# Kernel tuning notes

Measured on AMD Instinct MI355X. Metric: run time of the kernel, lower is better.

## Reference

```python
import jax, jax.numpy as jnp
import numpy as np

B, N, L = 32, 131072, 10
NUM_NEG_RATIO = 3
UP_CONF = 0.8
LO_CONF = 0.3
UP_IOU = 0.5
LO_IOU = 0.35
REG_COEFF = 1.0
MAX_OBJS = 10


def bboxes_iou_cxcywh(a, b):
    # a: [N,4], b: [L,4], boxes as (cx, cy, w, h) -> IoU matrix [N, L]
    tl = jnp.maximum(a[:, None, :2] - a[:, None, 2:] * 0.5,
                     b[None, :, :2] - b[None, :, 2:] * 0.5)
    br = jnp.minimum(a[:, None, :2] + a[:, None, 2:] * 0.5,
                     b[None, :, :2] + b[None, :, 2:] * 0.5)
    area_a = a[:, 2] * a[:, 3]
    area_b = b[:, 2] * b[:, 3]
    en = jnp.all(tl < br, axis=2)
    wh = br - tl
    area_i = wh[..., 0] * wh[..., 1] * en
    return area_i / (area_a[:, None] + area_b[None, :] - area_i)


def setup_inputs() -> dict:
    key = jax.random.key(0)
    k1, k2, k3, k4, k5 = jax.random.split(key, 5)
    logits = jax.random.normal(k1, (B, N)) * 2.0
    cxy = jax.random.uniform(k2, (B, N, 2), minval=0.0, maxval=4096.0)
    wh = jax.random.uniform(k3, (B, N, 2), minval=16.0, maxval=128.0)
    outputs = jnp.concatenate([cxy, wh, logits[..., None]], axis=-1)
    # plant L high-confidence priors per image whose boxes are jittered gt copies
    gidx = (jnp.arange(L) + 1) * 997
    outputs = outputs.at[:, gidx, 4].set(3.0)  # sigmoid(3) ~ 0.95 > 0.8
    jit_xy = jax.random.uniform(k4, (B, L, 2), minval=-3.0, maxval=3.0)
    jit_wh = jax.random.uniform(k5, (B, L, 2), minval=0.95, maxval=1.05)
    labels = jnp.concatenate([outputs[:, gidx, :2] + jit_xy,
                              outputs[:, gidx, 2:4] * jit_wh], axis=-1)
    labels = labels.at[:, 8:, 3].set(0.0)  # h==0 sentinel -> 8 valid gts per image
    return {"labels": labels, "outputs": outputs}


def _per_image(out, label):
    # out: [N,5], label: [L,4]
    logit = out[:, 4]
    conf = jax.nn.sigmoid(jax.lax.stop_gradient(logit))
    pcoords = jax.lax.stop_gradient(out[:, :4])
    h = label[:, 3]
    zero = h == 0.0
    last_idx = jnp.where(jnp.any(zero), jnp.argmax(zero), L)
    gt_valid = jnp.arange(L) < last_idx
    upper = conf > UP_CONF
    lower = conf < LO_CONF
    iou = bboxes_iou_cxcywh(pcoords, jax.lax.stop_gradient(label))  # [N,L]
    neg_inf = -jnp.inf
    iou_up = jnp.where(upper[:, None], iou, neg_inf)
    pos_ious = iou_up.max(axis=0)          # [L]
    pos_prior = iou_up.argmax(axis=0)      # [L] index into full prior dim
    neg_ious = jnp.where(lower[:, None], iou, neg_inf).max(axis=0)  # [L]
    gt_sel = gt_valid & (pos_ious >= UP_IOU)
    num_pos = gt_sel.sum()
    valid = (last_idx <= MAX_OBJS) & jnp.any(upper) & jnp.any(lower) & (num_pos > 0)
    # positive conf loss: BCEWithLogits target 1 -> softplus(-x)
    conf_pos = jnp.where(gt_sel, jax.nn.softplus(-logit[pos_prior]), 0.0).sum()
    # negatives (faithful to source quirk: gt indices index into thold_lower list)
    cs = jnp.cumsum(lower)
    match = lower[None, :] & (cs[None, :] == (jnp.arange(L) + 1)[:, None])  # [L,N]
    first_lower = jnp.argmax(match, axis=1)  # j-th lowest-index low-conf prior
    neg_cand = gt_valid & (neg_ious <= LO_IOU)
    cand_conf = jnp.where(neg_cand, conf[first_lower], neg_inf)
    rank = jnp.argsort(jnp.argsort(-cand_conf))
    neg_sel = neg_cand & (rank < NUM_NEG_RATIO * num_pos)
    # negative conf loss: target 0 -> softplus(x)
    conf_neg = jnp.where(neg_sel, jax.nn.softplus(logit[first_lower]), 0.0).sum()
    conf_loss = conf_pos + conf_neg
    pos_gt = label[:, :4]
    pred_box = out[pos_prior, :4]
    d = pred_box - pos_gt
    ad = jnp.abs(d)
    sl1 = jnp.where(ad < 1.0, 0.5 * d * d, ad - 0.5)
    max_lens = jnp.max(pos_gt[:, 2:4], axis=1, keepdims=True)
    max_lens = jnp.where(max_lens == 0.0, 1.0, max_lens)
    reg_loss = jnp.where(gt_sel[:, None], sl1 / max_lens, 0.0).sum()
    vf = valid.astype(out.dtype)
    return vf * conf_loss, vf * reg_loss, jnp.where(valid, num_pos, 0)


def reference(labels, outputs):
    conf_l, reg_l, npos = jax.vmap(_per_image)(outputs, labels)
    pos_selected = npos.sum()
    conf_loss = conf_l.sum()
    reg_loss = reg_l.sum()
    pos_f = jnp.maximum(pos_selected, 1).astype(outputs.dtype)
    ok = pos_selected >= 1
    total = jnp.where(ok, (conf_loss + REG_COEFF * reg_loss) / pos_f, 0.0)
    c = jnp.where(ok, conf_loss / pos_f, 0.0)
    r = jnp.where(ok, reg_loss / pos_f, 0.0)
    p = jnp.where(ok, pos_selected, 0).astype(outputs.dtype)
    return jnp.stack([total, c, r, p])
```

## Files before the change

kernel.cpp:

```cpp
#include <hip/hip_runtime.h>
#include <math.h>

#pragma clang fp contract(off)

#define BB 32
#define NN 131072
#define LL 10

constexpr int CHUNKS = 64;
constexpr int BLOCK  = 256;
constexpr int PER_CHUNK = NN / CHUNKS;
constexpr int GG = 4;
constexpr int ITERS = PER_CHUNK / (BLOCK * GG);

constexpr double UPPER_T =  1.3862943611198906;
constexpr double LOWER_T = -0.8472978603872034;

__device__ __forceinline__ unsigned int ordf(float f) {
    unsigned int b = __float_as_uint(f);
    return (b & 0x80000000u) ? ~b : (b | 0x80000000u);
}
__device__ __forceinline__ float unordf(unsigned int u) {
    unsigned int b = (u & 0x80000000u) ? (u & 0x7FFFFFFFu) : ~u;
    return __uint_as_float(b);
}
__device__ __forceinline__ unsigned long long shfl_xor_u64(unsigned long long v, int m) {
    int lo = __shfl_xor((int)(unsigned int)v, m, 64);
    int hi = __shfl_xor((int)(unsigned int)(v >> 32), m, 64);
    return ((unsigned long long)(unsigned int)hi << 32) | (unsigned long long)(unsigned int)lo;
}
__device__ __forceinline__ float softplusf(float x) {
    return fmaxf(x, 0.0f) + log1pf(expf(-fabsf(x)));
}

__global__ __launch_bounds__(BLOCK) void reduce_kernel(
    const float* __restrict__ outputs, const float* __restrict__ labels,
    unsigned long long* __restrict__ up_keys, unsigned int* __restrict__ lo_keys,
    unsigned int* __restrict__ flags)
{
    const int img   = blockIdx.x / CHUNKS;
    const int chunk = blockIdx.x % CHUNKS;
    const float* img_out = outputs + (size_t)img * NN * 5;

    __shared__ float sb[LL][5];
    __shared__ unsigned long long s_up[4][LL];
    __shared__ unsigned int s_lo[4][LL];
    __shared__ unsigned int s_flag;

    const int t = threadIdx.x;
    if (t < LL) {
        const float* lb = labels + ((size_t)img * LL + t) * 4;
        float cx = lb[0], cy = lb[1], w = lb[2], h = lb[3];
        sb[t][0] = cx - w * 0.5f;
        sb[t][1] = cy - h * 0.5f;
        sb[t][2] = cx + w * 0.5f;
        sb[t][3] = cy + h * 0.5f;
        sb[t][4] = w * h;
    }
    if (t == 0) s_flag = 0;
    __syncthreads();

    unsigned long long bu[LL];
    unsigned int bl[LL];
    #pragma unroll
    for (int j = 0; j < LL; ++j) { bu[j] = 0ull; bl[j] = 0u; }
    unsigned int myflag = 0;

    const int base = chunk * PER_CHUNK;
    #pragma unroll
    for (int it = 0; it < ITERS; ++it) {
        const int p0 = base + (it * BLOCK + t) * GG;
        const float4* src = (const float4*)(img_out + (size_t)p0 * 5);
        float4 v0 = src[0], v1 = src[1], v2 = src[2], v3 = src[3], v4 = src[4];
        float px[4] = { v0.x, v1.y, v2.z, v3.w };
        float py[4] = { v0.y, v1.z, v2.w, v4.x };
        float pw[4] = { v0.z, v1.w, v3.x, v4.y };
        float ph[4] = { v0.w, v2.x, v3.y, v4.z };
        float pl[4] = { v1.x, v2.y, v3.z, v4.w };
        #pragma unroll
        for (int g = 0; g < GG; ++g) {
            float logit = pl[g];
            bool up = (double)logit > UPPER_T;
            bool lo = (double)logit < LOWER_T;
            if (up) myflag |= 1u;
            if (lo) myflag |= 2u;
            if (up || lo) {
                float atlx = px[g] - pw[g] * 0.5f;
                float atly = py[g] - ph[g] * 0.5f;
                float abrx = px[g] + pw[g] * 0.5f;
                float abry = py[g] + ph[g] * 0.5f;
                float aa   = pw[g] * ph[g];
                unsigned int idx = (unsigned int)(p0 + g);
                #pragma unroll
                for (int j = 0; j < LL; ++j) {
                    float tlx = fmaxf(atlx, sb[j][0]);
                    float tly = fmaxf(atly, sb[j][1]);
                    float brx = fminf(abrx, sb[j][2]);
                    float bry = fminf(abry, sb[j][3]);
                    bool en = (tlx < brx) && (tly < bry);
                    float ai = en ? (brx - tlx) * (bry - tly) : 0.0f;
                    float iou = ai / (aa + sb[j][4] - ai);
                    unsigned int ub = ordf(iou);
                    if (up) {
                        unsigned long long key =
                            ((unsigned long long)ub << 32) | (unsigned long long)(0xFFFFFFFFu - idx);
                        if (key > bu[j]) bu[j] = key;
                    }
                    if (lo) {
                        if (ub > bl[j]) bl[j] = ub;
                    }
                }
            }
        }
    }

    const int wid = t >> 6;
    #pragma unroll
    for (int j = 0; j < LL; ++j) {
        unsigned long long v = bu[j];
        unsigned int u = bl[j];
        #pragma unroll
        for (int m = 1; m < 64; m <<= 1) {
            unsigned long long v2 = shfl_xor_u64(v, m);
            if (v2 > v) v = v2;
            unsigned int u2 = (unsigned int)__shfl_xor((int)u, m, 64);
            if (u2 > u) u = u2;
        }
        if ((t & 63) == 0) { s_up[wid][j] = v; s_lo[wid][j] = u; }
    }
    #pragma unroll
    for (int m = 1; m < 64; m <<= 1)
        myflag |= (unsigned int)__shfl_xor((int)myflag, m, 64);
    if ((t & 63) == 0) atomicOr(&s_flag, myflag);
    __syncthreads();

    if (t < LL) {
        unsigned long long m = s_up[0][t];
        #pragma unroll
        for (int w = 1; w < 4; ++w) if (s_up[w][t] > m) m = s_up[w][t];
        if (m) atomicMax(&up_keys[img * LL + t], m);
    } else if (t < 2 * LL) {
        int j = t - LL;
        unsigned int m = s_lo[0][j];
        #pragma unroll
        for (int w = 1; w < 4; ++w) if (s_lo[w][j] > m) m = s_lo[w][j];
        if (m) atomicMax(&lo_keys[img * LL + j], m);
    } else if (t == 2 * LL) {
        if (s_flag) atomicOr(&flags[img], s_flag);
    }
}

__global__ __launch_bounds__(64) void epilogue_kernel(
    const float* __restrict__ outputs, const float* __restrict__ labels,
    const unsigned long long* __restrict__ up_keys, const unsigned int* __restrict__ lo_keys,
    const unsigned int* __restrict__ flags,
    float* __restrict__ res_conf, float* __restrict__ res_reg, int* __restrict__ res_np)
{
    const int img  = blockIdx.x;
    const int lane = threadIdx.x;
    const float* po = outputs + (size_t)img * NN * 5;

    int fl[LL];
    #pragma unroll
    for (int j = 0; j < LL; ++j) fl[j] = 0;
    int cnt = 0;
    for (int k = 0; k < NN / 64 && cnt < LL; ++k) {
        float lg = po[(size_t)(k * 64 + lane) * 5 + 4];
        bool lo = (double)lg < LOWER_T;
        unsigned long long m = __ballot(lo);
        while (m && cnt < LL) {
            int b = __builtin_ctzll(m);
            fl[cnt++] = k * 64 + b;
            m &= (m - 1);
        }
    }
    if (lane != 0) return;

    float pos_iou[LL]; int pos_prior[LL]; float neg_iou[LL];
    for (int j = 0; j < LL; ++j) {
        unsigned long long key = up_keys[img * LL + j];
        if (key == 0ull) { pos_iou[j] = -INFINITY; pos_prior[j] = 0; }
        else {
            pos_iou[j]   = unordf((unsigned int)(key >> 32));
            pos_prior[j] = (int)(0xFFFFFFFFu - (unsigned int)key);
        }
        unsigned int lk = lo_keys[img * LL + j];
        neg_iou[j] = (lk == 0u) ? -INFINITY : unordf(lk);
    }

    const float* plab = labels + (size_t)img * LL * 4;
    int last_idx = LL;
    for (int j = 0; j < LL; ++j) {
        if (plab[j * 4 + 3] == 0.0f) { last_idx = j; break; }
    }

    bool gt_sel[LL]; int num_pos = 0;
    for (int j = 0; j < LL; ++j) {
        gt_sel[j] = (j < last_idx) && (pos_iou[j] >= 0.5f);
        num_pos += gt_sel[j] ? 1 : 0;
    }

    unsigned int f = flags[img];
    bool valid = (last_idx <= 10) && ((f & 1u) != 0) && ((f & 2u) != 0) && (num_pos > 0);

    float conf_pos = 0.0f;
    for (int j = 0; j < LL; ++j) {
        if (gt_sel[j]) {
            float lg = po[(size_t)pos_prior[j] * 5 + 4];
            conf_pos += softplusf(-lg);
        }
    }

    bool nc[LL]; float cl[LL];
    for (int j = 0; j < LL; ++j) {
        nc[j] = (j < last_idx) && (neg_iou[j] <= 0.35f);
        cl[j] = po[(size_t)fl[j] * 5 + 4];
    }

    float conf_neg = 0.0f;
    for (int j = 0; j < LL; ++j) {
        if (!nc[j]) continue;
        float cj = cl[j];
        int rank = 0;
        for (int k = 0; k < LL; ++k) {
            if (!nc[k]) continue;
            float ck = cl[k];
            if (ck > cj || (ck == cj && k < j)) rank++;
        }
        if (rank < 3 * num_pos) conf_neg += softplusf(cj);
    }

    float reg = 0.0f;
    for (int j = 0; j < LL; ++j) {
        if (!gt_sel[j]) continue;
        const float* pb = po + (size_t)pos_prior[j] * 5;
        const float* gb = plab + j * 4;
        float ml = fmaxf(gb[2], gb[3]);
        if (ml == 0.0f) ml = 1.0f;
        #pragma unroll
        for (int c = 0; c < 4; ++c) {
            float d  = pb[c] - gb[c];
            float ad = fabsf(d);
            float s  = (ad < 1.0f) ? 0.5f * d * d : (ad - 0.5f);
            reg += s / ml;
        }
    }

    res_conf[img] = valid ? (conf_pos + conf_neg) : 0.0f;
    res_reg[img]  = valid ? reg : 0.0f;
    res_np[img]   = valid ? num_pos : 0;
}

__global__ __launch_bounds__(64) void final_kernel(
    const float* __restrict__ res_conf, const float* __restrict__ res_reg,
    const int* __restrict__ res_np, float* __restrict__ out)
{
    if (threadIdx.x != 0 || blockIdx.x != 0) return;
    float cs = 0.0f, rs = 0.0f; int ps = 0;
    for (int i = 0; i < BB; ++i) {
        cs += res_conf[i];
        rs += res_reg[i];
        ps += res_np[i];
    }
    bool ok = ps >= 1;
    float pf = (float)(ps < 1 ? 1 : ps);
    out[0] = ok ? (cs + 1.0f * rs) / pf : 0.0f;
    out[1] = ok ? cs / pf : 0.0f;
    out[2] = ok ? rs / pf : 0.0f;
    out[3] = ok ? (float)ps : 0.0f;
}

extern "C" void kernel_launch(void* const* d_in, const int* in_sizes, int n_in,
                              void* d_out, int out_size, void* d_ws, size_t ws_size,
                              hipStream_t stream) {
    const float* labels  = (const float*)d_in[0];
    const float* outputs = (const float*)d_in[1];
    float* out = (float*)d_out;

    char* ws = (char*)d_ws;
    unsigned long long* up_keys = (unsigned long long*)(ws + 0);
    unsigned int*       lo_keys = (unsigned int*)(ws + 2560);
    unsigned int*       flags   = (unsigned int*)(ws + 3840);
    float*              res_conf= (float*)(ws + 3968);
    float*              res_reg = (float*)(ws + 4096);
    int*                res_np  = (int*)(ws + 4224);

    hipMemsetAsync(d_ws, 0, 4352, stream);

    hipLaunchKernelGGL(reduce_kernel, dim3(BB * CHUNKS), dim3(BLOCK), 0, stream,
                       outputs, labels, up_keys, lo_keys, flags);
    hipLaunchKernelGGL(epilogue_kernel, dim3(BB), dim3(64), 0, stream,
                       outputs, labels, up_keys, lo_keys, flags,
                       res_conf, res_reg, res_np);
    hipLaunchKernelGGL(final_kernel, dim3(1), dim3(64), 0, stream,
                       res_conf, res_reg, res_np, out);
}
```

Before: 167.0 us.

## Fuse reduce, epilogue and final kernels via last-block-done counter

Merges the three kernels into one. The last block to finish, detected with an atomic counter, runs the per-image epilogue across its four waves, using wave-parallel ballots and shuffles instead of a single lane, and then writes the final output. The inner IoU loop now tracks float max with an index and skips zero-overlap pairs, which reduces 64-bit key work. A new minimum-up-index key handles the case where the best IoU is zero. The trade-off is that the serial epilogue now runs inside a single block after the grid drains, including the first-lower-confidence scan over N for 32 images on only 4 waves.

```diff
diff --git a/kernel.cpp b/kernel.cpp
--- a/kernel.cpp
+++ b/kernel.cpp
@@ -12,6 +12,7 @@
 constexpr int PER_CHUNK = NN / CHUNKS;
 constexpr int GG = 4;
 constexpr int ITERS = PER_CHUNK / (BLOCK * GG);
+constexpr int GRID = BB * CHUNKS;
 
 constexpr double UPPER_T =  1.3862943611198906;
 constexpr double LOWER_T = -0.8472978603872034;
@@ -24,30 +25,39 @@
     unsigned int b = (u & 0x80000000u) ? (u & 0x7FFFFFFFu) : ~u;
     return __uint_as_float(b);
 }
-__device__ __forceinline__ unsigned long long shfl_xor_u64(unsigned long long v, int m) {
-    int lo = __shfl_xor((int)(unsigned int)v, m, 64);
-    int hi = __shfl_xor((int)(unsigned int)(v >> 32), m, 64);
-    return ((unsigned long long)(unsigned int)hi << 32) | (unsigned long long)(unsigned int)lo;
-}
 __device__ __forceinline__ float softplusf(float x) {
     return fmaxf(x, 0.0f) + log1pf(expf(-fabsf(x)));
 }
-
-__global__ __launch_bounds__(BLOCK) void reduce_kernel(
+__device__ __forceinline__ float wave_sum(float v) {
+    #pragma unroll
+    for (int m = 1; m < 64; m <<= 1) v += __shfl_xor(v, m, 64);
+    return v;
+}
+
+__global__ __launch_bounds__(BLOCK) void ohem_fused(
     const float* __restrict__ outputs, const float* __restrict__ labels,
     unsigned long long* __restrict__ up_keys, unsigned int* __restrict__ lo_keys,
-    unsigned int* __restrict__ flags)
+    unsigned int* __restrict__ flags, unsigned int* __restrict__ minup_keys,
+    unsigned int* __restrict__ counter, float* __restrict__ out)
 {
-    const int img   = blockIdx.x / CHUNKS;
-    const int chunk = blockIdx.x % CHUNKS;
+    const int bx    = blockIdx.x;
+    const int img   = bx >> 6;
+    const int chunk = bx & 63;
+    const int t     = threadIdx.x;
+    const int lane  = t & 63;
+    const int wid   = t >> 6;
     const float* img_out = outputs + (size_t)img * NN * 5;
 
     __shared__ float sb[LL][5];
-    __shared__ unsigned long long s_up[4][LL];
-    __shared__ unsigned int s_lo[4][LL];
-    __shared__ unsigned int s_flag;
-
-    const int t = threadIdx.x;
+    __shared__ float s_uf[4][LL];
+    __shared__ unsigned int s_ui[4][LL];
+    __shared__ float s_lf[4][LL];
+    __shared__ unsigned int s_mu[4];
+    __shared__ unsigned int s_fl[4];
+    __shared__ unsigned int s_last;
+    __shared__ float s_res[4][2];
+    __shared__ int s_np[4];
+
     if (t < LL) {
         const float* lb = labels + ((size_t)img * LL + t) * 4;
         float cx = lb[0], cy = lb[1], w = lb[2], h = lb[3];
@@ -57,19 +67,17 @@
         sb[t][3] = cy + h * 0.5f;
         sb[t][4] = w * h;
     }
-    if (t == 0) s_flag = 0;
-    __syncthreads();
-
-    unsigned long long bu[LL];
-    unsigned int bl[LL];
-    #pragma unroll
-    for (int j = 0; j < LL; ++j) { bu[j] = 0ull; bl[j] = 0u; }
+    __syncthreads();
+
+    float buf[LL]; unsigned int bui[LL]; float blf[LL];
+    #pragma unroll
+    for (int j = 0; j < LL; ++j) { buf[j] = 0.0f; bui[j] = 0xFFFFFFFFu; blf[j] = 0.0f; }
+    unsigned int minup  = 0xFFFFFFFFu;
     unsigned int myflag = 0;
 
-    const int base = chunk * PER_CHUNK;
     #pragma unroll
     for (int it = 0; it < ITERS; ++it) {
-        const int p0 = base + (it * BLOCK + t) * GG;
+        const int p0 = chunk * PER_CHUNK + (it * BLOCK + t) * GG;
         const float4* src = (const float4*)(img_out + (size_t)p0 * 5);
         float4 v0 = src[0], v1 = src[1], v2 = src[2], v3 = src[3], v4 = src[4];
         float px[4] = { v0.x, v1.y, v2.z, v3.w };
@@ -84,190 +92,193 @@
             bool lo = (double)logit < LOWER_T;
             if (up) myflag |= 1u;
             if (lo) myflag |= 2u;
+            unsigned int idx = (unsigned int)(p0 + g);
+            if (up && idx < minup) minup = idx;
             if (up || lo) {
                 float atlx = px[g] - pw[g] * 0.5f;
                 float atly = py[g] - ph[g] * 0.5f;
                 float abrx = px[g] + pw[g] * 0.5f;
                 float abry = py[g] + ph[g] * 0.5f;
                 float aa   = pw[g] * ph[g];
-                unsigned int idx = (unsigned int)(p0 + g);
                 #pragma unroll
                 for (int j = 0; j < LL; ++j) {
-                    float tlx = fmaxf(atlx, sb[j][0]);
-                    float tly = fmaxf(atly, sb[j][1]);
-                    float brx = fminf(abrx, sb[j][2]);
-                    float bry = fminf(abry, sb[j][3]);
-                    bool en = (tlx < brx) && (tly < bry);
-                    float ai = en ? (brx - tlx) * (bry - tly) : 0.0f;
-                    float iou = ai / (aa + sb[j][4] - ai);
-                    unsigned int ub = ordf(iou);
-                    if (up) {
-                        unsigned long long key =
-                            ((unsigned long long)ub << 32) | (unsigned long long)(0xFFFFFFFFu - idx);
-                        if (key > bu[j]) bu[j] = key;
-                    }
-                    if (lo) {
-                        if (ub > bl[j]) bl[j] = ub;
+                    float wj = fminf(abrx, sb[j][2]) - fmaxf(atlx, sb[j][0]);
+                    float hj = fminf(abry, sb[j][3]) - fmaxf(atly, sb[j][1]);
+                    wj = fmaxf(wj, 0.0f);
+                    hj = fmaxf(hj, 0.0f);
+                    float ai = wj * hj;
+                    if (ai > 0.0f) {
+                        float iou = ai / (aa + sb[j][4] - ai);
+                        if (up && iou > buf[j]) { buf[j] = iou; bui[j] = idx; }
+                        if (lo) blf[j] = fmaxf(blf[j], iou);
                     }
                 }
             }
         }
     }
 
-    const int wid = t >> 6;
     #pragma unroll
     for (int j = 0; j < LL; ++j) {
-        unsigned long long v = bu[j];
-        unsigned int u = bl[j];
+        float f = buf[j]; unsigned int i = bui[j];
+        float lf = blf[j];
         #pragma unroll
         for (int m = 1; m < 64; m <<= 1) {
-            unsigned long long v2 = shfl_xor_u64(v, m);
-            if (v2 > v) v = v2;
-            unsigned int u2 = (unsigned int)__shfl_xor((int)u, m, 64);
-            if (u2 > u) u = u2;
-        }
-        if ((t & 63) == 0) { s_up[wid][j] = v; s_lo[wid][j] = u; }
-    }
-    #pragma unroll
-    for (int m = 1; m < 64; m <<= 1)
+            float of = __shfl_xor(f, m, 64);
+            unsigned int oi = (unsigned int)__shfl_xor((int)i, m, 64);
+            if (of > f || (of == f && oi < i)) { f = of; i = oi; }
+            lf = fmaxf(lf, __shfl_xor(lf, m, 64));
+        }
+        if (lane == 0) { s_uf[wid][j] = f; s_ui[wid][j] = i; s_lf[wid][j] = lf; }
+    }
+    #pragma unroll
+    for (int m = 1; m < 64; m <<= 1) {
+        unsigned int om = (unsigned int)__shfl_xor((int)minup, m, 64);
+        if (om < minup) minup = om;
         myflag |= (unsigned int)__shfl_xor((int)myflag, m, 64);
-    if ((t & 63) == 0) atomicOr(&s_flag, myflag);
+    }
+    if (lane == 0) { s_mu[wid] = minup; s_fl[wid] = myflag; }
     __syncthreads();
 
     if (t < LL) {
-        unsigned long long m = s_up[0][t];
-        #pragma unroll
-        for (int w = 1; w < 4; ++w) if (s_up[w][t] > m) m = s_up[w][t];
-        if (m) atomicMax(&up_keys[img * LL + t], m);
+        float f = s_uf[0][t]; unsigned int i = s_ui[0][t];
+        #pragma unroll
+        for (int w2 = 1; w2 < 4; ++w2) {
+            float of = s_uf[w2][t]; unsigned int oi = s_ui[w2][t];
+            if (of > f || (of == f && oi < i)) { f = of; i = oi; }
+        }
+        if (f > 0.0f) {
+            unsigned long long key = ((unsigned long long)ordf(f) << 32)
+                                   | (unsigned long long)(0xFFFFFFFFu - i);
+            atomicMax(&up_keys[img * LL + t], key);
+        }
     } else if (t < 2 * LL) {
         int j = t - LL;
-        unsigned int m = s_lo[0][j];
-        #pragma unroll
-        for (int w = 1; w < 4; ++w) if (s_lo[w][j] > m) m = s_lo[w][j];
-        if (m) atomicMax(&lo_keys[img * LL + j], m);
+        float f = fmaxf(fmaxf(s_lf[0][j], s_lf[1][j]), fmaxf(s_lf[2][j], s_lf[3][j]));
+        if (f > 0.0f) atomicMax(&lo_keys[img * LL + j], ordf(f));
     } else if (t == 2 * LL) {
-        if (s_flag) atomicOr(&flags[img], s_flag);
-    }
-}
-
-__global__ __launch_bounds__(64) void epilogue_kernel(
-    const float* __restrict__ outputs, const float* __restrict__ labels,
-    const unsigned long long* __restrict__ up_keys, const unsigned int* __restrict__ lo_keys,
-    const unsigned int* __restrict__ flags,
-    float* __restrict__ res_conf, float* __restrict__ res_reg, int* __restrict__ res_np)
-{
-    const int img  = blockIdx.x;
-    const int lane = threadIdx.x;
-    const float* po = outputs + (size_t)img * NN * 5;
-
-    int fl[LL];
-    #pragma unroll
-    for (int j = 0; j < LL; ++j) fl[j] = 0;
-    int cnt = 0;
-    for (int k = 0; k < NN / 64 && cnt < LL; ++k) {
-        float lg = po[(size_t)(k * 64 + lane) * 5 + 4];
-        bool lo = (double)lg < LOWER_T;
-        unsigned long long m = __ballot(lo);
-        while (m && cnt < LL) {
-            int b = __builtin_ctzll(m);
-            fl[cnt++] = k * 64 + b;
-            m &= (m - 1);
-        }
-    }
-    if (lane != 0) return;
-
-    float pos_iou[LL]; int pos_prior[LL]; float neg_iou[LL];
-    for (int j = 0; j < LL; ++j) {
-        unsigned long long key = up_keys[img * LL + j];
-        if (key == 0ull) { pos_iou[j] = -INFINITY; pos_prior[j] = 0; }
-        else {
-            pos_iou[j]   = unordf((unsigned int)(key >> 32));
-            pos_prior[j] = (int)(0xFFFFFFFFu - (unsigned int)key);
-        }
-        unsigned int lk = lo_keys[img * LL + j];
-        neg_iou[j] = (lk == 0u) ? -INFINITY : unordf(lk);
-    }
-
-    const float* plab = labels + (size_t)img * LL * 4;
-    int last_idx = LL;
-    for (int j = 0; j < LL; ++j) {
-        if (plab[j * 4 + 3] == 0.0f) { last_idx = j; break; }
-    }
-
-    bool gt_sel[LL]; int num_pos = 0;
-    for (int j = 0; j < LL; ++j) {
-        gt_sel[j] = (j < last_idx) && (pos_iou[j] >= 0.5f);
-        num_pos += gt_sel[j] ? 1 : 0;
-    }
-
-    unsigned int f = flags[img];
-    bool valid = (last_idx <= 10) && ((f & 1u) != 0) && ((f & 2u) != 0) && (num_pos > 0);
-
-    float conf_pos = 0.0f;
-    for (int j = 0; j < LL; ++j) {
-        if (gt_sel[j]) {
-            float lg = po[(size_t)pos_prior[j] * 5 + 4];
-            conf_pos += softplusf(-lg);
-        }
-    }
-
-    bool nc[LL]; float cl[LL];
-    for (int j = 0; j < LL; ++j) {
-        nc[j] = (j < last_idx) && (neg_iou[j] <= 0.35f);
-        cl[j] = po[(size_t)fl[j] * 5 + 4];
-    }
-
-    float conf_neg = 0.0f;
-    for (int j = 0; j < LL; ++j) {
-        if (!nc[j]) continue;
-        float cj = cl[j];
+        unsigned int fl2 = s_fl[0] | s_fl[1] | s_fl[2] | s_fl[3];
+        if (fl2) atomicOr(&flags[img], fl2);
+    } else if (t == 2 * LL + 1) {
+        unsigned int mu = s_mu[0];
+        if (s_mu[1] < mu) mu = s_mu[1];
+        if (s_mu[2] < mu) mu = s_mu[2];
+        if (s_mu[3] < mu) mu = s_mu[3];
+        if (mu != 0xFFFFFFFFu) atomicMax(&minup_keys[img], ~mu);
+    }
+
+    __syncthreads();
+    if (t == 0) {
+        __threadfence();
+        unsigned int old = atomicAdd(counter, 1u);
+        s_last = (old == (unsigned int)(GRID - 1)) ? 1u : 0u;
+    }
+    __syncthreads();
+    if (s_last == 0u) return;
+    __threadfence();
+
+    float acc_conf = 0.0f, acc_reg = 0.0f; int acc_np = 0;
+    for (int ii = 0; ii < BB / 4; ++ii) {
+        const int im = wid + 4 * ii;
+        const float* po   = outputs + (size_t)im * NN * 5;
+        const float* plab = labels + (size_t)im * LL * 4;
+
+        int fl[LL];
+        #pragma unroll
+        for (int j = 0; j < LL; ++j) fl[j] = 0;
+        int cnt = 0;
+        for (int k = 0; k < NN / 64 && cnt < LL; ++k) {
+            float lg = po[(size_t)(k * 64 + lane) * 5 + 4];
+            unsigned long long m = __ballot((double)lg < LOWER_T);
+            while (m && cnt < LL) {
+                int b = __builtin_ctzll(m);
+                fl[cnt++] = k * 64 + b;
+                m &= (m - 1);
+            }
+        }
+
+        unsigned int fimg0 = 0, muk0 = 0;
+        if (lane == 0) {
+            fimg0 = atomicOr(&flags[im], 0u);
+            muk0  = atomicMax(&minup_keys[im], 0u);
+        }
+        unsigned int fimg = (unsigned int)__shfl((int)fimg0, 0, 64);
+        unsigned int muk  = (unsigned int)__shfl((int)muk0, 0, 64);
+        bool any_up = (fimg & 1u) != 0u;
+        bool any_lo = (fimg & 2u) != 0u;
+
+        unsigned long long ukey = 0ull; unsigned int lkey = 0u;
+        float g0 = 0.0f, g1 = 0.0f, g2 = 0.0f, g3 = 1.0f;
+        if (lane < LL) {
+            ukey = atomicMax(&up_keys[im * LL + lane], 0ull);
+            lkey = atomicMax(&lo_keys[im * LL + lane], 0u);
+            g0 = plab[lane * 4 + 0];
+            g1 = plab[lane * 4 + 1];
+            g2 = plab[lane * 4 + 2];
+            g3 = plab[lane * 4 + 3];
+        }
+
+        unsigned long long zb = __ballot(lane < LL && g3 == 0.0f) & 0x3FFull;
+        int last_idx = zb ? __builtin_ctzll(zb) : LL;
+
+        float piou; unsigned int pprior;
+        if (ukey != 0ull) {
+            piou = unordf((unsigned int)(ukey >> 32));
+            pprior = 0xFFFFFFFFu - (unsigned int)ukey;
+        } else if (any_up) {
+            piou = 0.0f; pprior = ~muk;
+        } else {
+            piou = -INFINITY; pprior = 0u;
+        }
+        float niou = lkey ? unordf(lkey) : (any_lo ? 0.0f : -INFINITY);
+
+        bool gt_sel = (lane < last_idx) && (piou >= 0.5f);
+        int np = __builtin_popcountll(__ballot(gt_sel) & 0x3FFull);
+        bool valid = any_up && any_lo && (np > 0);
+
+        float cp = 0.0f, rg = 0.0f;
+        if (gt_sel) {
+            const float* pb = po + (size_t)pprior * 5;
+            cp = softplusf(-pb[4]);
+            float ml = fmaxf(g2, g3);
+            if (ml == 0.0f) ml = 1.0f;
+            float gv[4] = { g0, g1, g2, g3 };
+            #pragma unroll
+            for (int c = 0; c < 4; ++c) {
+                float d  = pb[c] - gv[c];
+                float ad = fabsf(d);
+                float s  = (ad < 1.0f) ? 0.5f * d * d : (ad - 0.5f);
+                rg += s / ml;
+            }
+        }
+
+        bool nc = (lane < last_idx) && (niou <= 0.35f);
+        unsigned long long ncm = __ballot(nc) & 0x3FFull;
+        float cl = (lane < LL) ? po[(size_t)fl[lane] * 5 + 4] : 0.0f;
         int rank = 0;
+        #pragma unroll
         for (int k = 0; k < LL; ++k) {
-            if (!nc[k]) continue;
-            float ck = cl[k];
-            if (ck > cj || (ck == cj && k < j)) rank++;
-        }
-        if (rank < 3 * num_pos) conf_neg += softplusf(cj);
-    }
-
-    float reg = 0.0f;
-    for (int j = 0; j < LL; ++j) {
-        if (!gt_sel[j]) continue;
-        const float* pb = po + (size_t)pos_prior[j] * 5;
-        const float* gb = plab + j * 4;
-        float ml = fmaxf(gb[2], gb[3]);
-        if (ml == 0.0f) ml = 1.0f;
-        #pragma unroll
-        for (int c = 0; c < 4; ++c) {
-            float d  = pb[c] - gb[c];
-            float ad = fabsf(d);
-            float s  = (ad < 1.0f) ? 0.5f * d * d : (ad - 0.5f);
-            reg += s / ml;
-        }
-    }
-
-    res_conf[img] = valid ? (conf_pos + conf_neg) : 0.0f;
-    res_reg[img]  = valid ? reg : 0.0f;
-    res_np[img]   = valid ? num_pos : 0;
-}
-
-__global__ __launch_bounds__(64) void final_kernel(
-    const float* __restrict__ res_conf, const float* __restrict__ res_reg,
-    const int* __restrict__ res_np, float* __restrict__ out)
-{
-    if (threadIdx.x != 0 || blockIdx.x != 0) return;
-    float cs = 0.0f, rs = 0.0f; int ps = 0;
-    for (int i = 0; i < BB; ++i) {
-        cs += res_conf[i];
-        rs += res_reg[i];
-        ps += res_np[i];
-    }
-    bool ok = ps >= 1;
-    float pf = (float)(ps < 1 ? 1 : ps);
-    out[0] = ok ? (cs + 1.0f * rs) / pf : 0.0f;
-    out[1] = ok ? cs / pf : 0.0f;
-    out[2] = ok ? rs / pf : 0.0f;
-    out[3] = ok ? (float)ps : 0.0f;
+            float ck = __shfl(cl, k, 64);
+            if (((ncm >> k) & 1ull) && (ck > cl || (ck == cl && k < lane))) rank++;
+        }
+        float cn = (nc && rank < 3 * np) ? softplusf(cl) : 0.0f;
+
+        float conf_im = wave_sum(cp + cn);
+        float reg_im  = wave_sum(rg);
+        if (valid) { acc_conf += conf_im; acc_reg += reg_im; acc_np += np; }
+    }
+    if (lane == 0) { s_res[wid][0] = acc_conf; s_res[wid][1] = acc_reg; s_np[wid] = acc_np; }
+    __syncthreads();
+    if (t == 0) {
+        float cs = 0.0f, rs = 0.0f; int ps = 0;
+        #pragma unroll
+        for (int w2 = 0; w2 < 4; ++w2) { cs += s_res[w2][0]; rs += s_res[w2][1]; ps += s_np[w2]; }
+        bool ok = ps >= 1;
+        float pf = (float)(ps < 1 ? 1 : ps);
+        out[0] = ok ? (cs + 1.0f * rs) / pf : 0.0f;
+        out[1] = ok ? cs / pf : 0.0f;
+        out[2] = ok ? rs / pf : 0.0f;
+        out[3] = ok ? (float)ps : 0.0f;
+    }
 }
 
 extern "C" void kernel_launch(void* const* d_in, const int* in_sizes, int n_in,
@@ -279,19 +290,13 @@
 
     char* ws = (char*)d_ws;
     unsigned long long* up_keys = (unsigned long long*)(ws + 0);
-    unsigned int*       lo_keys = (unsigned int*)(ws + 2560);
-    unsigned int*       flags   = (unsigned int*)(ws + 3840);
-    float*              res_conf= (float*)(ws + 3968);
-    float*              res_reg = (float*)(ws + 4096);
-    int*                res_np  = (int*)(ws + 4224);
-
-    hipMemsetAsync(d_ws, 0, 4352, stream);
-
-    hipLaunchKernelGGL(reduce_kernel, dim3(BB * CHUNKS), dim3(BLOCK), 0, stream,
-                       outputs, labels, up_keys, lo_keys, flags);
-    hipLaunchKernelGGL(epilogue_kernel, dim3(BB), dim3(64), 0, stream,
-                       outputs, labels, up_keys, lo_keys, flags,
-                       res_conf, res_reg, res_np);
-    hipLaunchKernelGGL(final_kernel, dim3(1), dim3(64), 0, stream,
-                       res_conf, res_reg, res_np, out);
-}
+    unsigned int* lo_keys    = (unsigned int*)(ws + 2560);
+    unsigned int* flags      = (unsigned int*)(ws + 3840);
+    unsigned int* minup_keys = (unsigned int*)(ws + 3968);
+    unsigned int* counter    = (unsigned int*)(ws + 4096);
+
+    hipMemsetAsync(ws, 0, 4104, stream);
+    hipLaunchKernelGGL(ohem_fused, dim3(GRID), dim3(BLOCK), 0, stream,
+                       outputs, labels, up_keys, lo_keys, flags, minup_keys,
+                       counter, out);
+}
```

Measured after the change: 219.8 us. +31.6%, slower.
